# Kernel tuning notes

Measured on AMD Instinct MI355X. Metric: run time of the kernel, lower is better.

## Reference

```python
import jax, jax.numpy as jnp
import numpy as np

N = 768      # n_proto (number of class prototypes)
D = 128      # trans_feat_num
H = D // 16  # edge-MLP hidden = 8
A = 312      # semantic attribute dim
INIT_TEMP = 0.1
VTEMP = 10.0
STEMP = 10.0
EPS = 1e-8


def _layer_norm(x, g, b, eps=1e-5):
    m = x.mean(-1, keepdims=True)
    v = ((x - m) ** 2).mean(-1, keepdims=True)
    return (x - m) / jnp.sqrt(v + eps) * g + b


def _instance_norm_rows(x, eps=1e-5):
    # torch InstanceNorm1d on 2D input: unbatched (C, L) -> normalize each row, no affine
    m = x.mean(-1, keepdims=True)
    v = ((x - m) ** 2).mean(-1, keepdims=True)
    return (x - m) / jnp.sqrt(v + eps)


def _init_edge(x, temp):
    # pairwise cosine similarity + row softmax
    nrm = jnp.linalg.norm(x, axis=1)
    sim = (x @ x.T) / jnp.maximum(nrm[:, None] * nrm[None, :], EPS)
    return jax.nn.softmax(sim / temp, axis=-1)


def _edge_update(proto, last_edge, W1, b1, W2, b2, temp):
    n, d = proto.shape
    # O(n^2) pairwise squared differences  -> [n*n, d]
    feat = ((proto[:, None, :] - proto[None, :, :]) ** 2).reshape(n * n, d)
    h = jax.nn.relu(_instance_norm_rows(feat @ W1.T + b1))  # [n*n, H]
    e = jnp.tanh(h @ W2.T + b2).reshape(n, n)
    return jax.nn.softmax(e * (last_edge + EPS) / temp, axis=-1)


def _node_update(proto, last_edge, edge, W, b, g, beta):
    extra = last_edge @ proto          # cross-modal message (dist_injection)
    p = edge @ proto                   # same-modal aggregation
    return jax.nn.relu(_layer_norm((p + extra) @ W.T + b, g, beta)) + p


def setup_inputs() -> dict:
    key = jax.random.key(0)
    ks = jax.random.split(key, 9)
    rn = lambda k, shape, s=1.0: jax.random.normal(k, shape, dtype=jnp.float32) * s
    return {
        "visual_proto": rn(ks[0], (N, D)),
        "semantic_proto": rn(ks[1], (N, D)),
        "attribute": rn(ks[2], (N, A)),
        "Wvn": rn(ks[3], (D, D), 0.08), "bvn": jnp.zeros((D,), jnp.float32),
        "gvn": jnp.ones((D,), jnp.float32), "betavn": jnp.zeros((D,), jnp.float32),
        "Wve1": rn(ks[4], (H, D), 0.1), "bve1": jnp.zeros((H,), jnp.float32),
        "Wve2": rn(ks[5], (1, H), 0.3), "bve2": jnp.zeros((1,), jnp.float32),
        "Wsn": rn(ks[6], (D, D), 0.08), "bsn": jnp.zeros((D,), jnp.float32),
        "gsn": jnp.ones((D,), jnp.float32), "betasn": jnp.zeros((D,), jnp.float32),
        "Wse1": rn(ks[7], (H, D), 0.1), "bse1": jnp.zeros((H,), jnp.float32),
        "Wse2": rn(ks[8], (1, H), 0.3), "bse2": jnp.zeros((1,), jnp.float32),
    }


def reference(visual_proto, semantic_proto, attribute,
              Wvn, bvn, gvn, betavn, Wve1, bve1, Wve2, bve2,
              Wsn, bsn, gsn, betasn, Wse1, bse1, Wse2, bse2):
    ve = _init_edge(visual_proto, INIT_TEMP)
    se = _init_edge(attribute, INIT_TEMP)
    vp = _node_update(visual_proto, se, ve, Wvn, bvn, gvn, betavn)
    ve2 = _edge_update(vp, ve, Wve1, bve1, Wve2, bve2, VTEMP)
    sp = _node_update(semantic_proto, ve2, se, Wsn, bsn, gsn, betasn)
    se2 = _edge_update(sp, se, Wse1, bse1, Wse2, bse2, STEMP)
    return vp, sp, ve2, se2
```

## Files before the change

### kernel.cpp

```cpp
#include <hip/hip_runtime.h>
#include <math.h>

#define NN 768
#define DD 128
#define AA 312
#define HH 8
#define CEPS 1e-8f

typedef __attribute__((ext_vector_type(8))) short s8b;
typedef __attribute__((ext_vector_type(4))) float f4v;

__device__ __forceinline__ float wave_sum(float v) {
    #pragma unroll
    for (int o = 32; o; o >>= 1) v += __shfl_down(v, o, 64);
    return v;
}
__device__ __forceinline__ float wave_max(float v) {
    #pragma unroll
    for (int o = 32; o; o >>= 1) v = fmaxf(v, __shfl_down(v, o, 64));
    return v;
}
__device__ __forceinline__ unsigned short f2bf(float f) {
    unsigned u = __float_as_uint(f);
    u += 0x7FFFu + ((u >> 16) & 1u);
    return (unsigned short)(u >> 16);
}

template <int COLS>
__device__ void gram_tile(const float* __restrict__ A, float invtemp, float* __restrict__ sim,
                          int i0, int j0, int tid, float* As, float* Bs) {
    const int tx = tid & 15, ty = tid >> 4;
    const int lr = tid >> 3, lc4 = (tid & 7) * 4;
    float acc00 = 0.f, acc01 = 0.f, acc10 = 0.f, acc11 = 0.f;
    float si0 = 0.f, si1 = 0.f, sj0 = 0.f, sj1 = 0.f;
    for (int kc = 0; kc < COLS; kc += 32) {
        float4 av, bv;
        if (kc + lc4 + 4 <= COLS) {
            av = *(const float4*)(A + (size_t)(i0 + lr) * COLS + kc + lc4);
            bv = *(const float4*)(A + (size_t)(j0 + lr) * COLS + kc + lc4);
        } else {
            float ta[4], tb[4];
            #pragma unroll
            for (int l = 0; l < 4; ++l) {
                int c = kc + lc4 + l;
                ta[l] = (c < COLS) ? A[(size_t)(i0 + lr) * COLS + c] : 0.f;
                tb[l] = (c < COLS) ? A[(size_t)(j0 + lr) * COLS + c] : 0.f;
            }
            av = make_float4(ta[0], ta[1], ta[2], ta[3]);
            bv = make_float4(tb[0], tb[1], tb[2], tb[3]);
        }
        __syncthreads();
        As[(lc4 + 0) * 34 + lr] = av.x; As[(lc4 + 1) * 34 + lr] = av.y;
        As[(lc4 + 2) * 34 + lr] = av.z; As[(lc4 + 3) * 34 + lr] = av.w;
        Bs[(lc4 + 0) * 34 + lr] = bv.x; Bs[(lc4 + 1) * 34 + lr] = bv.y;
        Bs[(lc4 + 2) * 34 + lr] = bv.z; Bs[(lc4 + 3) * 34 + lr] = bv.w;
        __syncthreads();
        #pragma unroll
        for (int k = 0; k < 32; ++k) {
            float2 aa = *(const float2*)&As[k * 34 + 2 * ty];
            float2 bb = *(const float2*)&Bs[k * 34 + 2 * tx];
            acc00 = fmaf(aa.x, bb.x, acc00);
            acc01 = fmaf(aa.x, bb.y, acc01);
            acc10 = fmaf(aa.y, bb.x, acc10);
            acc11 = fmaf(aa.y, bb.y, acc11);
            si0 = fmaf(aa.x, aa.x, si0);
            si1 = fmaf(aa.y, aa.y, si1);
            sj0 = fmaf(bb.x, bb.x, sj0);
            sj1 = fmaf(bb.y, bb.y, sj1);
        }
    }
    const float ni0 = sqrtf(si0), ni1 = sqrtf(si1);
    const float nj0 = sqrtf(sj0), nj1 = sqrtf(sj1);
    float* s0 = sim + (size_t)(i0 + 2 * ty) * NN + j0 + 2 * tx;
    float* s1 = s0 + NN;
    s0[0] = acc00 / fmaxf(ni0 * nj0, CEPS) * invtemp;
    s0[1] = acc01 / fmaxf(ni0 * nj1, CEPS) * invtemp;
    s1[0] = acc10 / fmaxf(ni1 * nj0, CEPS) * invtemp;
    s1[1] = acc11 / fmaxf(ni1 * nj1, CEPS) * invtemp;
}

__global__ __launch_bounds__(256) void gram_prep_kernel(
    const float* __restrict__ visual, const float* __restrict__ attribute,
    const float* __restrict__ Wvn, const float* __restrict__ Wsn, float* __restrict__ simv,
    float* __restrict__ sima, float* __restrict__ WvnT, float* __restrict__ WsnT) {
    __shared__ __align__(16) float smem[2176];
    const int tid = threadIdx.x;
    const int task = blockIdx.x;
    if (task < 576) {
        gram_tile<DD>(visual, 10.f, simv, (task / 24) * 32, (task % 24) * 32, tid, smem,
                      smem + 1088);
    } else if (task < 1152) {
        const int rem = task - 576;
        gram_tile<AA>(attribute, 10.f, sima, (rem / 24) * 32, (rem % 24) * 32, tid, smem,
                      smem + 1088);
    } else {
        const int u = task - 1152;
        const float* S = (u >= 16) ? Wsn : Wvn;
        float* Dt = (u >= 16) ? WsnT : WvnT;
        const int tile = u & 15;
        const int c0 = (tile & 3) * 32, r0 = (tile >> 2) * 32;
        const int tx = tid & 31, ty = tid >> 5;
        #pragma unroll
        for (int rr = ty; rr < 32; rr += 8)
            smem[rr * 33 + tx] = S[(size_t)(r0 + rr) * DD + c0 + tx];
        __syncthreads();
        #pragma unroll
        for (int rr = ty; rr < 32; rr += 8)
            Dt[(size_t)(c0 + rr) * DD + r0 + tx] = smem[tx * 33 + rr];
    }
}

__device__ void softmax_row_g(const float* __restrict__ vr, float* __restrict__ dst, int tid,
                              float* red) {
    float v0 = vr[tid], v1 = vr[tid + 256], v2 = vr[tid + 512];
    float m = wave_max(fmaxf(fmaxf(v0, v1), v2));
    if ((tid & 63) == 0) red[tid >> 6] = m;
    __syncthreads();
    m = fmaxf(fmaxf(red[0], red[1]), fmaxf(red[2], red[3]));
    float e0 = __expf(v0 - m), e1 = __expf(v1 - m), e2 = __expf(v2 - m);
    float sw = wave_sum(e0 + e1 + e2);
    if ((tid & 63) == 0) red[4 + (tid >> 6)] = sw;
    __syncthreads();
    const float s = red[4] + red[5] + red[6] + red[7];
    const float inv = 1.f / s;
    dst[tid] = e0 * inv;
    dst[tid + 256] = e1 * inv;
    dst[tid + 512] = e2 * inv;
}

__global__ __launch_bounds__(256) void softmax_all_kernel(const float* __restrict__ simv,
                                                          const float* __restrict__ sima,
                                                          float* __restrict__ ve,
                                                          float* __restrict__ se) {
    __shared__ float red[8];
    const int task = blockIdx.x;
    const float* src = (task < NN) ? simv + (size_t)task * NN : sima + (size_t)(task - NN) * NN;
    float* dst = (task < NN) ? ve + (size_t)task * NN : se + (size_t)(task - NN) * NN;
    softmax_row_g(src, dst, threadIdx.x, red);
}

__device__ void block_softmax768(float* buf, int tid, float* red) {
    const int w = tid >> 6, lane = tid & 63;
    float v0 = buf[tid];
    float v1 = (tid < NN - 512) ? buf[tid + 512] : -3.4e38f;
    float m = wave_max(fmaxf(v0, v1));
    if (lane == 0) red[w] = m;
    __syncthreads();
    m = red[0];
    #pragma unroll
    for (int i = 1; i < 8; ++i) m = fmaxf(m, red[i]);
    float e0 = __expf(v0 - m);
    float e1 = (tid < NN - 512) ? __expf(v1 - m) : 0.f;
    float sw = wave_sum(e0 + e1);
    if (lane == 0) red[8 + w] = sw;
    __syncthreads();
    float s = 0.f;
    #pragma unroll
    for (int i = 0; i < 8; ++i) s += red[8 + i];
    const float inv = 1.f / s;
    buf[tid] = e0 * inv;
    if (tid < NN - 512) buf[tid + 512] = e1 * inv;
    __syncthreads();
}

__global__ __launch_bounds__(512) void node_kernel(
    const float* __restrict__ P, const float* __restrict__ Ep, const float* __restrict__ Ex,
    const float* __restrict__ WT, const float* __restrict__ b, const float* __restrict__ g,
    const float* __restrict__ beta, float* __restrict__ out, const float* __restrict__ W1e,
    short* __restrict__ outb, float* __restrict__ cvec) {
    __shared__ __align__(16) float ep[2][NN], ex[2][NN];
    __shared__ __align__(16) float pp[4][2][DD], xx[4][2][DD];
    __shared__ __align__(16) float qs[2][DD], tps[2][2][DD];
    __shared__ float red[16];
    const int i0 = blockIdx.x * 2;
    const int tid = threadIdx.x;
    const int s = (tid >> 7) & 3, d = tid & 127;
    #pragma unroll
    for (int r = 0; r < 2; ++r)
        for (int k = tid; k < NN; k += 512) {
            ep[r][k] = Ep[(size_t)(i0 + r) * NN + k];
            ex[r][k] = Ex[(size_t)(i0 + r) * NN + k];
        }
    __syncthreads();
    float p0 = 0.f, x0 = 0.f, p1 = 0.f, x1 = 0.f;
    const int kb = s * 192;
    #pragma unroll 4
    for (int kk = 0; kk < 192; ++kk) {
        const int k = kb + kk;
        const float pv = P[(size_t)k * DD + d];
        p0 = fmaf(ep[0][k], pv, p0);
        x0 = fmaf(ex[0][k], pv, x0);
        p1 = fmaf(ep[1][k], pv, p1);
        x1 = fmaf(ex[1][k], pv, x1);
    }
    pp[s][0][d] = p0; xx[s][0][d] = x0;
    pp[s][1][d] = p1; xx[s][1][d] = x1;
    __syncthreads();
    const int rr = (tid >> 7) & 1;
    float preg = 0.f;
    if (tid < 256) {
        float p = pp[0][rr][d] + pp[1][rr][d] + pp[2][rr][d] + pp[3][rr][d];
        float x = xx[0][rr][d] + xx[1][rr][d] + xx[2][rr][d] + xx[3][rr][d];
        qs[rr][d] = p + x;
        preg = p;
    }
    __syncthreads();
    {
        const int sc = tid >> 8, rr2 = (tid >> 7) & 1;
        float t = (sc == 0) ? b[d] : 0.f;
        const int c0 = sc * 64;
        #pragma unroll 4
        for (int c = c0; c < c0 + 64; ++c) t = fmaf(qs[rr2][c], WT[(size_t)c * DD + d], t);
        tps[sc][rr2][d] = t;
    }
    __syncthreads();
    float tval = 0.f;
    if (tid < 256) tval = tps[0][rr][d] + tps[1][rr][d];
    float sm = wave_sum(tid < 256 ? tval : 0.f);
    if ((tid & 63) == 0) red[tid >> 6] = sm;
    __syncthreads();
    if (tid < 256) tval -= (red[2 * rr] + red[2 * rr + 1]) * (1.f / DD);
    float s2 = wave_sum(tid < 256 ? tval * tval : 0.f);
    if ((tid & 63) == 0) red[8 + (tid >> 6)] = s2;
    __syncthreads();
    if (tid < 256) {
        const float var = (red[8 + 2 * rr] + red[8 + 2 * rr + 1]) * (1.f / DD);
        const float ln = tval * rsqrtf(var + 1e-5f) * g[d] + beta[d];
        const float val = fmaxf(ln, 0.f) + preg;
        out[(size_t)(i0 + rr) * DD + d] = val;
        outb[(size_t)(i0 + rr) * DD + d] = (short)f2bf(val);
        qs[rr][d] = val;
    }
    __syncthreads();
    if (tid < 256) {
        const int row = tid >> 7, r = (tid >> 4) & 7, l16 = tid & 15;
        float ssum = 0.f;
        #pragma unroll
        for (int t = 0; t < 8; ++t) {
            const int k = l16 + 16 * t;
            const float pv = qs[row][k];
            ssum = fmaf(W1e[r * DD + k], pv * pv, ssum);
        }
        #pragma unroll
        for (int o = 8; o; o >>= 1) ssum += __shfl_down(ssum, o, 16);
        if (l16 == 0) cvec[(size_t)(i0 + row) * HH + r] = ssum;
    }
}

__global__ __launch_bounds__(512) void edge_fused_kernel(
    const float* __restrict__ PR, const short* __restrict__ PRb, const float* __restrict__ cvec,
    const float* __restrict__ Elast, const float* __restrict__ W1, const float* __restrict__ b1,
    const float* __restrict__ W2, const float* __restrict__ b2, float invtemp,
    float* __restrict__ out) {
    const int i0 = blockIdx.x * 2;
    const int tid = threadIdx.x;
    const int lane = tid & 63, wave = tid >> 6;
    __shared__ __align__(16) float pi[2][DD];
    __shared__ __align__(16) float w1s[HH * DD];
    __shared__ __align__(16) short a_sw[4 * 64 * 8];
    __shared__ __align__(16) float Ls[2][NN];
    __shared__ float red[16];
    if (tid < 256) {
        pi[tid >> 7][tid & 127] = PR[(size_t)(i0 + (tid >> 7)) * DD + (tid & 127)];
        ((float4*)w1s)[tid] = ((const float4*)W1)[tid];
    }
    __syncthreads();
    if (tid < 256) {
        const int t = tid >> 6, m = lane & 15, q2 = lane >> 4;
        const int il = m >> 3, r = m & 7;
        const int kb = t * 32 + q2 * 8;
        s8b av;
        #pragma unroll
        for (int e = 0; e < 8; ++e)
            av[e] = (short)f2bf(pi[il][kb + e] * w1s[r * DD + kb + e]);
        *(s8b*)&a_sw[(t * 64 + lane) * 8] = av;
    }
    __syncthreads();
    s8b af[4];
    #pragma unroll
    for (int t = 0; t < 4; ++t) af[t] = *(const s8b*)&a_sw[(t * 64 + lane) * 8];
    const int q = lane >> 4, n = lane & 15;
    const int rbase = (q & 1) * 4;
    const int il = q >> 1;
    const float4 ci4 = *(const float4*)&cvec[(size_t)(i0 + il) * HH + rbase];
    const float4 b14 = *(const float4*)&b1[rbase];
    const float4 w24 = *(const float4*)&W2[rbase];
    const float b2s = b2[0];
    #pragma unroll
    for (int s = 0; s < 6; ++s) {
        const int j = wave * 96 + s * 16 + n;
        f4v acc = {0.f, 0.f, 0.f, 0.f};
        #pragma unroll
        for (int t = 0; t < 4; ++t) {
            const s8b bf = *(const s8b*)(PRb + (size_t)j * DD + t * 32 + q * 8);
            acc = __builtin_amdgcn_mfma_f32_16x16x32_bf16(af[t], bf, acc, 0, 0, 0);
        }
        const float4 cj = *(const float4*)&cvec[(size_t)j * HH + rbase];
        float z[4];
        z[0] = ci4.x + cj.x - 2.f * acc[0] + b14.x;
        z[1] = ci4.y + cj.y - 2.f * acc[1] + b14.y;
        z[2] = ci4.z + cj.z - 2.f * acc[2] + b14.z;
        z[3] = ci4.w + cj.w - 2.f * acc[3] + b14.w;
        float s1 = z[0] + z[1] + z[2] + z[3];
        float s2 = z[0] * z[0] + z[1] * z[1] + z[2] * z[2] + z[3] * z[3];
        s1 += __shfl_xor(s1, 16, 64);
        s2 += __shfl_xor(s2, 16, 64);
        const float mean = s1 * (1.f / HH);
        const float var = fmaxf(s2 * (1.f / HH) - mean * mean, 0.f);
        const float istd = rsqrtf(var + 1e-5f);
        float a2 = 0.f;
        a2 = fmaf(fmaxf((z[0] - mean) * istd, 0.f), w24.x, a2);
        a2 = fmaf(fmaxf((z[1] - mean) * istd, 0.f), w24.y, a2);
        a2 = fmaf(fmaxf((z[2] - mean) * istd, 0.f), w24.z, a2);
        a2 = fmaf(fmaxf((z[3] - mean) * istd, 0.f), w24.w, a2);
        a2 += __shfl_xor(a2, 16, 64);
        const float tv = tanhf(a2 + b2s);
        const float lv = Elast[(size_t)(i0 + il) * NN + j];
        if ((q & 1) == 0) Ls[il][j] = tv * (lv + CEPS) * invtemp;
    }
    __syncthreads();
    block_softmax768(Ls[0], tid, red);
    block_softmax768(Ls[1], tid, red);
    float* d0 = out + (size_t)i0 * NN;
    float* d1 = out + (size_t)(i0 + 1) * NN;
    d0[tid] = Ls[0][tid];
    d1[tid] = Ls[1][tid];
    if (tid < NN - 512) {
        d0[tid + 512] = Ls[0][tid + 512];
        d1[tid + 512] = Ls[1][tid + 512];
    }
}

extern "C" void kernel_launch(void* const* d_in, const int* in_sizes, int n_in, void* d_out,
                              int out_size, void* d_ws, size_t ws_size, hipStream_t stream) {
    const float* visual    = (const float*)d_in[0];
    const float* semantic  = (const float*)d_in[1];
    const float* attribute = (const float*)d_in[2];
    const float* Wvn  = (const float*)d_in[3];
    const float* bvn  = (const float*)d_in[4];
    const float* gvn  = (const float*)d_in[5];
    const float* betavn = (const float*)d_in[6];
    const float* Wve1 = (const float*)d_in[7];
    const float* bve1 = (const float*)d_in[8];
    const float* Wve2 = (const float*)d_in[9];
    const float* bve2 = (const float*)d_in[10];
    const float* Wsn  = (const float*)d_in[11];
    const float* bsn  = (const float*)d_in[12];
    const float* gsn  = (const float*)d_in[13];
    const float* betasn = (const float*)d_in[14];
    const float* Wse1 = (const float*)d_in[15];
    const float* bse1 = (const float*)d_in[16];
    const float* Wse2 = (const float*)d_in[17];
    const float* bse2 = (const float*)d_in[18];

    float* out = (float*)d_out;
    float* vp  = out;
    float* sp  = out + 98304;
    float* ve2 = out + 196608;
    float* se2 = out + 786432;

    float* ws    = (float*)d_ws;
    float* simv  = ws;
    float* sima  = ws + 589824;
    float* ve    = ws + 1179648;
    float* se    = ws + 1769472;
    float* WvnT  = ws + 2949120;
    float* WsnT  = ws + 2965504;
    float* cvec1 = ws + 2981888;
    float* cvec2 = ws + 2988032;
    short* vpb   = (short*)(ws + 2994176);
    short* spb   = (short*)(ws + 3043328);

    gram_prep_kernel<<<1184, 256, 0, stream>>>(visual, attribute, Wvn, Wsn, simv, sima, WvnT,
                                               WsnT);
    softmax_all_kernel<<<1536, 256, 0, stream>>>(simv, sima, ve, se);
    node_kernel<<<NN / 2, 512, 0, stream>>>(visual, ve, se, WvnT, bvn, gvn, betavn, vp, Wve1,
                                            vpb, cvec1);
    edge_fused_kernel<<<NN / 2, 512, 0, stream>>>(vp, vpb, cvec1, ve, Wve1, bve1, Wve2, bve2,
                                                  0.1f, ve2);
    node_kernel<<<NN / 2, 512, 0, stream>>>(semantic, se, ve2, WsnT, bsn, gsn, betasn, sp, Wse1,
                                            spb, cvec2);
    edge_fused_kernel<<<NN / 2, 512, 0, stream>>>(sp, spb, cvec2, se, Wse1, bse1, Wse2, bse2,
                                                  0.1f, se2);
}
```

Baseline: 194.5 us.

## Fuse init-edge row softmax into node and edge kernels, drop softmax pass

Removes the standalone softmax kernel over the two 768x768 similarity matrices and the ve/se workspace buffers. Each node and edge kernel now loads the raw similarity rows it needs into shared memory and applies the row softmax in place before using them. This saves one launch and a full write-then-read of two N×N matrices, but the softmax is recomputed in up to three consumer kernels. It also adds block barriers and more shared memory in the edge kernel, which may lower occupancy.

Measured after the change: 197.6 us. Within noise of the previous version (+1.6%).

```diff
diff --git a/kernel.cpp b/kernel.cpp
--- a/kernel.cpp
+++ b/kernel.cpp
@@ -110,35 +110,6 @@
     }
 }
 
-__device__ void softmax_row_g(const float* __restrict__ vr, float* __restrict__ dst, int tid,
-                              float* red) {
-    float v0 = vr[tid], v1 = vr[tid + 256], v2 = vr[tid + 512];
-    float m = wave_max(fmaxf(fmaxf(v0, v1), v2));
-    if ((tid & 63) == 0) red[tid >> 6] = m;
-    __syncthreads();
-    m = fmaxf(fmaxf(red[0], red[1]), fmaxf(red[2], red[3]));
-    float e0 = __expf(v0 - m), e1 = __expf(v1 - m), e2 = __expf(v2 - m);
-    float sw = wave_sum(e0 + e1 + e2);
-    if ((tid & 63) == 0) red[4 + (tid >> 6)] = sw;
-    __syncthreads();
-    const float s = red[4] + red[5] + red[6] + red[7];
-    const float inv = 1.f / s;
-    dst[tid] = e0 * inv;
-    dst[tid + 256] = e1 * inv;
-    dst[tid + 512] = e2 * inv;
-}
-
-__global__ __launch_bounds__(256) void softmax_all_kernel(const float* __restrict__ simv,
-                                                          const float* __restrict__ sima,
-                                                          float* __restrict__ ve,
-                                                          float* __restrict__ se) {
-    __shared__ float red[8];
-    const int task = blockIdx.x;
-    const float* src = (task < NN) ? simv + (size_t)task * NN : sima + (size_t)(task - NN) * NN;
-    float* dst = (task < NN) ? ve + (size_t)task * NN : se + (size_t)(task - NN) * NN;
-    softmax_row_g(src, dst, threadIdx.x, red);
-}
-
 __device__ void block_softmax768(float* buf, int tid, float* red) {
     const int w = tid >> 6, lane = tid & 63;
     float v0 = buf[tid];
@@ -163,8 +134,9 @@
     __syncthreads();
 }
 
+template <bool SMEP, bool SMEX>
 __global__ __launch_bounds__(512) void node_kernel(
-    const float* __restrict__ P, const float* __restrict__ Ep, const float* __restrict__ Ex,
+    const float* __restrict__ P, const float* __restrict__ EpSrc, const float* __restrict__ ExSrc,
     const float* __restrict__ WT, const float* __restrict__ b, const float* __restrict__ g,
     const float* __restrict__ beta, float* __restrict__ out, const float* __restrict__ W1e,
     short* __restrict__ outb, float* __restrict__ cvec) {
@@ -175,13 +147,19 @@
     const int i0 = blockIdx.x * 2;
     const int tid = threadIdx.x;
     const int s = (tid >> 7) & 3, d = tid & 127;
-    #pragma unroll
-    for (int r = 0; r < 2; ++r)
-        for (int k = tid; k < NN; k += 512) {
-            ep[r][k] = Ep[(size_t)(i0 + r) * NN + k];
-            ex[r][k] = Ex[(size_t)(i0 + r) * NN + k];
-        }
-    __syncthreads();
+    if (tid < 384) {
+        ((float4*)ep)[tid] = ((const float4*)(EpSrc + (size_t)i0 * NN))[tid];
+        ((float4*)ex)[tid] = ((const float4*)(ExSrc + (size_t)i0 * NN))[tid];
+    }
+    __syncthreads();
+    if (SMEP) {
+        block_softmax768(ep[0], tid, red);
+        block_softmax768(ep[1], tid, red);
+    }
+    if (SMEX) {
+        block_softmax768(ex[0], tid, red);
+        block_softmax768(ex[1], tid, red);
+    }
     float p0 = 0.f, x0 = 0.f, p1 = 0.f, x1 = 0.f;
     const int kb = s * 192;
     #pragma unroll 4
@@ -249,7 +227,7 @@
 
 __global__ __launch_bounds__(512) void edge_fused_kernel(
     const float* __restrict__ PR, const short* __restrict__ PRb, const float* __restrict__ cvec,
-    const float* __restrict__ Elast, const float* __restrict__ W1, const float* __restrict__ b1,
+    const float* __restrict__ ELraw, const float* __restrict__ W1, const float* __restrict__ b1,
     const float* __restrict__ W2, const float* __restrict__ b2, float invtemp,
     float* __restrict__ out) {
     const int i0 = blockIdx.x * 2;
@@ -259,12 +237,17 @@
     __shared__ __align__(16) float w1s[HH * DD];
     __shared__ __align__(16) short a_sw[4 * 64 * 8];
     __shared__ __align__(16) float Ls[2][NN];
+    __shared__ __align__(16) float Els[2][NN];
     __shared__ float red[16];
     if (tid < 256) {
         pi[tid >> 7][tid & 127] = PR[(size_t)(i0 + (tid >> 7)) * DD + (tid & 127)];
         ((float4*)w1s)[tid] = ((const float4*)W1)[tid];
     }
-    __syncthreads();
+    if (tid < 384)
+        ((float4*)Els)[tid] = ((const float4*)(ELraw + (size_t)i0 * NN))[tid];
+    __syncthreads();
+    block_softmax768(Els[0], tid, red);
+    block_softmax768(Els[1], tid, red);
     if (tid < 256) {
         const int t = tid >> 6, m = lane & 15, q2 = lane >> 4;
         const int il = m >> 3, r = m & 7;
@@ -315,7 +298,7 @@
         a2 = fmaf(fmaxf((z[3] - mean) * istd, 0.f), w24.w, a2);
         a2 += __shfl_xor(a2, 16, 64);
         const float tv = tanhf(a2 + b2s);
-        const float lv = Elast[(size_t)(i0 + il) * NN + j];
+        const float lv = Els[il][j];
         if ((q & 1) == 0) Ls[il][j] = tv * (lv + CEPS) * invtemp;
     }
     __syncthreads();
@@ -362,8 +345,6 @@
     float* ws    = (float*)d_ws;
     float* simv  = ws;
     float* sima  = ws + 589824;
-    float* ve    = ws + 1179648;
-    float* se    = ws + 1769472;
     float* WvnT  = ws + 2949120;
     float* WsnT  = ws + 2965504;
     float* cvec1 = ws + 2981888;
@@ -373,13 +354,12 @@
 
     gram_prep_kernel<<<1184, 256, 0, stream>>>(visual, attribute, Wvn, Wsn, simv, sima, WvnT,
                                                WsnT);
-    softmax_all_kernel<<<1536, 256, 0, stream>>>(simv, sima, ve, se);
-    node_kernel<<<NN / 2, 512, 0, stream>>>(visual, ve, se, WvnT, bvn, gvn, betavn, vp, Wve1,
-                                            vpb, cvec1);
-    edge_fused_kernel<<<NN / 2, 512, 0, stream>>>(vp, vpb, cvec1, ve, Wve1, bve1, Wve2, bve2,
+    node_kernel<true, true><<<NN / 2, 512, 0, stream>>>(visual, simv, sima, WvnT, bvn, gvn,
+                                                        betavn, vp, Wve1, vpb, cvec1);
+    edge_fused_kernel<<<NN / 2, 512, 0, stream>>>(vp, vpb, cvec1, simv, Wve1, bve1, Wve2, bve2,
                                                   0.1f, ve2);
-    node_kernel<<<NN / 2, 512, 0, stream>>>(semantic, se, ve2, WsnT, bsn, gsn, betasn, sp, Wse1,
-                                            spb, cvec2);
-    edge_fused_kernel<<<NN / 2, 512, 0, stream>>>(sp, spb, cvec2, se, Wse1, bse1, Wse2, bse2,
+    node_kernel<true, false><<<NN / 2, 512, 0, stream>>>(semantic, sima, ve2, WsnT, bsn, gsn,
+                                                         betasn, sp, Wse1, spb, cvec2);
+    edge_fused_kernel<<<NN / 2, 512, 0, stream>>>(sp, spb, cvec2, sima, Wse1, bse1, Wse2, bse2,
                                                   0.1f, se2);
 }
```
